# Kernel tuning notes

Measured on AMD Instinct MI355X. Metric: run time of the kernel, lower is better.

The kernel has to match this reference:

```python
import jax, jax.numpy as jnp
import numpy as np

NUM_HEADS = 12


def _apply_rope(t, cos, sin):
    # t: [B, N, H, Dh]; cos/sin: [N, Dh//2]
    B, N, H, Dh = t.shape
    tr = t.reshape(B, N, H, Dh // 2, 2)
    a, b = tr[..., 0], tr[..., 1]
    c = cos[None, :, None, :]
    s = sin[None, :, None, :]
    out_r = a * c - b * s
    out_i = a * s + b * c
    return jnp.stack([out_r, out_i], axis=-1).reshape(B, N, H, Dh)


def setup_inputs() -> dict:
    key = jax.random.key(0)
    ks = jax.random.split(key, 6)
    B, N, C, H = 4, 2048, 768, NUM_HEADS
    Dh = C // H
    x = jax.random.normal(ks[0], (B, N, C), dtype=jnp.float32)
    # RoPE frequencies (standard theta=10000 schedule) -> cos/sin of shape [N, Dh//2]
    inv_freq = 1.0 / (10000.0 ** (np.arange(0, Dh, 2, dtype=np.float32) / Dh))
    t = np.arange(N, dtype=np.float32)
    ang = np.outer(t, inv_freq)  # [N, Dh//2]
    freqs_cos = jnp.asarray(np.cos(ang))
    freqs_sin = jnp.asarray(np.sin(ang))
    # additive causal mask, broadcastable to [B, H, N, N]
    neg = jnp.float32(-1e9)
    mask = jnp.where(jnp.tril(jnp.ones((N, N), dtype=bool)), 0.0, neg)[None, None]
    w_qkv = jax.random.normal(ks[1], (3 * C, C), dtype=jnp.float32) * 0.02
    w_proj = jax.random.normal(ks[2], (C, C), dtype=jnp.float32) * 0.02
    b_proj = jnp.zeros((C,), dtype=jnp.float32)
    return {"x": x, "freqs_cos": freqs_cos, "freqs_sin": freqs_sin,
            "mask": mask, "w_qkv": w_qkv, "w_proj": w_proj, "b_proj": b_proj}


def reference(x, freqs_cos, freqs_sin, mask, w_qkv, w_proj, b_proj):
    B, N, C = x.shape
    H = NUM_HEADS
    Dh = C // H
    scale = Dh ** -0.5
    qkv = x @ w_qkv.T                               # [B, N, 3C] (qkv_bias=False)
    qkv = qkv.reshape(B, N, 3, H, Dh)
    q, k, v = qkv[:, :, 0], qkv[:, :, 1], qkv[:, :, 2]   # [B, N, H, Dh]
    q = _apply_rope(q, freqs_cos, freqs_sin)
    k = _apply_rope(k, freqs_cos, freqs_sin)
    q = q.transpose(0, 2, 1, 3)                     # [B, H, N, Dh]
    k = k.transpose(0, 2, 1, 3)
    v = v.transpose(0, 2, 1, 3)
    attn = jnp.einsum('bhqd,bhkd->bhqk', q, k) * scale
    attn = attn + mask
    attn = jax.nn.softmax(attn, axis=-1)
    out = jnp.einsum('bhqk,bhkd->bhqd', attn, v)    # [B, H, N, Dh]
    out = out.transpose(0, 2, 1, 3).reshape(B, N, C)
    return out @ w_proj.T + b_proj
```

## Files before the change

### kernel.cpp

```cpp
#include <hip/hip_runtime.h>
#include <hip/hip_bf16.h>

#define DEVI static __device__ __forceinline__

typedef __attribute__((ext_vector_type(8))) short bf16x8;
typedef __attribute__((ext_vector_type(4))) float f32x4;
typedef __attribute__((ext_vector_type(16))) float f32x16;
typedef __attribute__((ext_vector_type(4))) int i32x4;

constexpr int Bc = 4, Nc = 2048, Cc = 768, Hc = 12, Dhc = 64;
constexpr int Mc = Bc * Nc;
constexpr int K3c = 3 * Cc;

DEVI unsigned int f2bf(float f) {
  unsigned int u = __float_as_uint(f);
  return (u + 0x7fffu + ((u >> 16) & 1u)) >> 16;
}
DEVI float bf2f(unsigned int u) { return __uint_as_float(u << 16); }

DEVI unsigned int cvtpk_bf16(float lo, float hi_) {
  unsigned int r;
  asm("v_cvt_pk_bf16_f32 %0, %1, %2" : "=v"(r) : "v"(lo), "v"(hi_));
  return r;
}

#if __has_builtin(__builtin_amdgcn_exp2f)
#define EXP2(x) __builtin_amdgcn_exp2f(x)
#else
#define EXP2(x) exp2f(x)
#endif

#define GLOAD_LDS(g, l)                                                              \
  __builtin_amdgcn_global_load_lds((const __attribute__((address_space(1))) void*)(g), \
                                   (__attribute__((address_space(3))) void*)(l), 16, 0, 0)

DEVI unsigned int rope_pair(unsigned int w, float c, float s) {
  const float a = bf2f(w & 0xffffu), b_ = bf2f(w >> 16);
  return f2bf(a * c - b_ * s) | (f2bf(a * s + b_ * c) << 16);
}

__global__ __launch_bounds__(256) void cvt_f32_bf16(const float* __restrict__ in,
                                                    unsigned short* __restrict__ out, int n8) {
  const int i = blockIdx.x * 256 + threadIdx.x;
  if (i >= n8) return;
  const f32x4 a = *((const f32x4*)in + (size_t)i * 2);
  const f32x4 b = *((const f32x4*)in + (size_t)i * 2 + 1);
  i32x4 v;
  v.x = (int)(f2bf(a.x) | (f2bf(a.y) << 16));
  v.y = (int)(f2bf(a.z) | (f2bf(a.w) << 16));
  v.z = (int)(f2bf(b.x) | (f2bf(b.y) << 16));
  v.w = (int)(f2bf(b.z) | (f2bf(b.w) << 16));
  *((i32x4*)out + i) = v;
}

template <int OBF16>
__global__ __launch_bounds__(256) void gemm_bt16(const unsigned short* __restrict__ Ap,
                                                 const unsigned short* __restrict__ Wp,
                                                 void* __restrict__ Cp,
                                                 const float* __restrict__ bias,
                                                 int Nout, int Kdim) {
  __shared__ unsigned short As[128 * 64];
  __shared__ unsigned short Bs[128 * 64];
  const int tid = threadIdx.x;
  const int bn = blockIdx.x, bm = blockIdx.y;
  const int m0 = bm * 128, n0 = bn * 128;
  const int w = tid >> 6, lane = tid & 63;
  const int wr = w >> 1, wc = w & 1;
  const int lr = lane & 15, lg = lane >> 4;
  const int r = lane >> 3, slot = lane & 7;

  f32x4 acc[4][4];
#pragma unroll
  for (int i = 0; i < 4; ++i)
#pragma unroll
    for (int j = 0; j < 4; ++j) acc[i][j] = f32x4{0.f, 0.f, 0.f, 0.f};

  for (int kt = 0; kt < Kdim; kt += 64) {
    __syncthreads();
#pragma unroll
    for (int c = 0; c < 4; ++c) {
      const int i = (w << 2) + c;
      const int row = (i << 3) + r;
      const unsigned short* ga = Ap + (size_t)(m0 + row) * Kdim + kt + ((slot ^ r) << 3);
      GLOAD_LDS(ga, As + (i << 9));
      const unsigned short* gb = Wp + (size_t)(n0 + row) * Kdim + kt + ((slot ^ r) << 3);
      GLOAD_LDS(gb, Bs + (i << 9));
    }
    __syncthreads();

    bf16x8 af[4][2], bfr[4][2];
#pragma unroll
    for (int mf = 0; mf < 4; ++mf) {
      const int row = wr * 64 + mf * 16 + lr;
#pragma unroll
      for (int kk = 0; kk < 2; ++kk)
        af[mf][kk] = *(const bf16x8*)&As[row * 64 + (((kk * 4 + lg) ^ (row & 7)) * 8)];
    }
#pragma unroll
    for (int nf = 0; nf < 4; ++nf) {
      const int row = wc * 64 + nf * 16 + lr;
#pragma unroll
      for (int kk = 0; kk < 2; ++kk)
        bfr[nf][kk] = *(const bf16x8*)&Bs[row * 64 + (((kk * 4 + lg) ^ (row & 7)) * 8)];
    }
#pragma unroll
    for (int mf = 0; mf < 4; ++mf)
#pragma unroll
      for (int nf = 0; nf < 4; ++nf)
#pragma unroll
        for (int kk = 0; kk < 2; ++kk)
          acc[mf][nf] = __builtin_amdgcn_mfma_f32_16x16x32_bf16(af[mf][kk], bfr[nf][kk],
                                                                acc[mf][nf], 0, 0, 0);
  }

#pragma unroll
  for (int mf = 0; mf < 4; ++mf) {
#pragma unroll
    for (int nf = 0; nf < 4; ++nf) {
      const int col = n0 + wc * 64 + nf * 16 + lr;
#pragma unroll
      for (int rg = 0; rg < 4; ++rg) {
        const int rowg = m0 + wr * 64 + mf * 16 + lg * 4 + rg;
        const float v = acc[mf][nf][rg];
        if constexpr (OBF16) {
          ((unsigned short*)Cp)[(size_t)rowg * Nout + col] = (unsigned short)f2bf(v);
        } else {
          ((float*)Cp)[(size_t)rowg * Nout + col] = v + bias[col];
        }
      }
    }
  }
}

__global__ __launch_bounds__(256) void rope_q(const unsigned short* __restrict__ qkv,
                                              const float* __restrict__ fcos,
                                              const float* __restrict__ fsin,
                                              unsigned short* __restrict__ Qo) {
  constexpr float KL = 0.18033688011112042f;
  const int idx = blockIdx.x * 256 + threadIdx.x;
  if (idx >= Bc * Nc * Hc * 32) return;
  const int dp = idx & 31;
  const int t = idx >> 5;
  const int h = t % Hc;
  const int bn = t / Hc;
  const int n = bn & (Nc - 1);
  const int b = bn >> 11;
  const size_t qoff = (size_t)bn * 3 * Cc + h * 64 + dp * 2;
  const unsigned int qp = *(const unsigned int*)&qkv[qoff];
  const float c = fcos[n * 32 + dp], s = fsin[n * 32 + dp];
  const float qa = bf2f(qp & 0xffffu), qb = bf2f(qp >> 16);
  const unsigned int qo = f2bf(KL * (qa * c - qb * s)) | (f2bf(KL * (qa * s + qb * c)) << 16);
  const size_t o = ((size_t)((b * Hc + h) * Nc) + n) * Dhc + dp * 2;
  *(unsigned int*)&Qo[o] = qo;
}

__global__ __launch_bounds__(256) void pack_kv(const unsigned short* __restrict__ qkv,
                                               const float* __restrict__ fcos,
                                               const float* __restrict__ fsin,
                                               unsigned short* __restrict__ Kc,
                                               unsigned short* __restrict__ Vc) {
  __shared__ unsigned short kt[64 * 72];
  __shared__ unsigned short vt[64 * 72];
  const int nt = blockIdx.x, bh = blockIdx.y;
  const int b = bh / Hc, h = bh % Hc;
  const int n0 = nt * 64;
  const int tid = threadIdx.x;
  const int nl = tid >> 3, slot = tid & 7;

#pragma unroll
  for (int it = 0; it < 2; ++it) {
    const int n = it * 32 + nl;
    const size_t base = (size_t)(b * Nc + n0 + n) * K3c + h * 64 + slot * 8;
    i32x4 vv = *(const i32x4*)&qkv[base + 2 * Cc];
    *(i32x4*)&vt[n * 72 + slot * 8] = vv;
    i32x4 kv = *(const i32x4*)&qkv[base + Cc];
    const f32x4 cv = *(const f32x4*)&fcos[(n0 + n) * 32 + slot * 4];
    const f32x4 sv = *(const f32x4*)&fsin[(n0 + n) * 32 + slot * 4];
    i32x4 ko;
    ko.x = (int)rope_pair((unsigned int)kv.x, cv.x, sv.x);
    ko.y = (int)rope_pair((unsigned int)kv.y, cv.y, sv.y);
    ko.z = (int)rope_pair((unsigned int)kv.z, cv.z, sv.z);
    ko.w = (int)rope_pair((unsigned int)kv.w, cv.w, sv.w);
    *(i32x4*)&kt[n * 72 + slot * 8] = ko;
  }
  __syncthreads();

#pragma unroll
  for (int it = 0; it < 2; ++it) {
    const int task = it * 256 + tid;
    const int g = task >> 6;
    const int d = task & 63;
    unsigned short tmpv[8];
#pragma unroll
    for (int j = 0; j < 8; ++j) tmpv[j] = vt[(g * 8 + j) * 72 + d];
    *(i32x4*)&Vc[(((size_t)bh * 256 + (n0 >> 3) + g) * 64 + d) * 8] = *(const i32x4*)tmpv;
    *(i32x4*)&Kc[(((size_t)bh * 8 + g) * Nc + n0 + d) * 8] = *(const i32x4*)&kt[d * 72 + g * 8];
  }
}

__global__ __launch_bounds__(64, 4) void attn_fwd(const unsigned short* __restrict__ Qp,
                                                  const unsigned short* __restrict__ Kcp,
                                                  const unsigned short* __restrict__ Vcp,
                                                  unsigned short* __restrict__ Op) {
  const int id = blockIdx.x;
  const int x8 = id & 7;
  const int rr_ = id >> 3;
  const int seg = 63 - rr_ / 6;
  const int bh = x8 + ((rr_ % 6) << 3);
  const int lane = threadIdx.x;
  const int qc = lane & 31, hi = lane >> 5;
  const int qw0 = seg * 32;
  const int qrow = qw0 + qc;
  const int qwmax = qw0 + 31;
  const unsigned short* Kcb = Kcp + (size_t)bh * (8 * Nc * 8);
  const unsigned short* Vcb = Vcp + (size_t)bh * (256 * 64 * 8);

  bf16x8 qf[4];
  {
    const unsigned short* qptr = Qp + ((size_t)bh * Nc + qrow) * 64 + hi * 8;
#pragma unroll
    for (int ks = 0; ks < 4; ++ks) qf[ks] = *(const bf16x8*)(qptr + ks * 16);
  }

  f32x16 oacc[2];
#pragma unroll
  for (int dt = 0; dt < 2; ++dt)
#pragma unroll
    for (int j = 0; j < 16; ++j) oacc[dt][j] = 0.f;
  float m_run = -1e30f, l_run = 0.f;

  for (int k0 = 0; k0 <= qwmax; k0 += 64) {
    bf16x8 kf[2][4];
#pragma unroll
    for (int f = 0; f < 2; ++f)
#pragma unroll
      for (int ks = 0; ks < 4; ++ks)
        kf[f][ks] = *(const bf16x8*)&Kcb[(((2 * ks + hi) * Nc) + k0 + f * 32 + qc) * 8];

    bf16x8 vf[2][4];
#pragma unroll
    for (int dt = 0; dt < 2; ++dt)
#pragma unroll
      for (int ks = 0; ks < 4; ++ks)
        vf[dt][ks] = *(const bf16x8*)&Vcb[(((k0 >> 3) + 2 * ks + hi) * 64 + dt * 32 + qc) * 8];

    f32x16 sacc[2];
#pragma unroll
    for (int f = 0; f < 2; ++f)
#pragma unroll
      for (int j = 0; j < 16; ++j) sacc[f][j] = 0.f;
#pragma unroll
    for (int f = 0; f < 2; ++f)
#pragma unroll
      for (int ks = 0; ks < 4; ++ks)
        sacc[f] = __builtin_amdgcn_mfma_f32_32x32x16_bf16(kf[f][ks], qf[ks], sacc[f], 0, 0, 0);

    if (k0 + 63 > qw0) {
#pragma unroll
      for (int f = 0; f < 2; ++f)
#pragma unroll
        for (int rr = 0; rr < 16; ++rr) {
          const int kvi = k0 + f * 32 + (rr & 3) + ((rr >> 2) << 3) + (hi << 2);
          if (kvi > qrow) sacc[f][rr] = -1e30f;
        }
    }

    float mx[16];
#pragma unroll
    for (int j = 0; j < 16; ++j) mx[j] = fmaxf(sacc[0][j], sacc[1][j]);
#pragma unroll
    for (int st = 8; st >= 1; st >>= 1)
#pragma unroll
      for (int j = 0; j < st; ++j) mx[j] = fmaxf(mx[j], mx[j + st]);
    const float pmax = fmaxf(mx[0], __shfl_xor(mx[0], 32, 64));

    if (!__all(pmax - m_run <= 11.5f)) {
      const float m_new = fmaxf(m_run, pmax);
      const float rs = EXP2(m_run - m_new);
      l_run *= rs;
#pragma unroll
      for (int dt = 0; dt < 2; ++dt)
#pragma unroll
        for (int j = 0; j < 16; ++j) oacc[dt][j] *= rs;
      m_run = m_new;
    }

    float p[32];
#pragma unroll
    for (int f = 0; f < 2; ++f)
#pragma unroll
      for (int rr = 0; rr < 16; ++rr) p[f * 16 + rr] = EXP2(sacc[f][rr] - m_run);

    float ts[16];
#pragma unroll
    for (int j = 0; j < 16; ++j) ts[j] = p[j] + p[16 + j];
#pragma unroll
    for (int st = 8; st >= 1; st >>= 1)
#pragma unroll
      for (int j = 0; j < st; ++j) ts[j] += ts[j + st];
    l_run += ts[0] + __shfl_xor(ts[0], 32, 64);

    unsigned int pw[2][8];
#pragma unroll
    for (int f = 0; f < 2; ++f) {
#pragma unroll
      for (int j = 0; j < 8; ++j)
        pw[f][j] = cvtpk_bf16(p[f * 16 + 2 * j], p[f * 16 + 2 * j + 1]);
      asm volatile("v_permlane32_swap_b32 %0, %1" : "+v"(pw[f][0]), "+v"(pw[f][2]));
      asm volatile("v_permlane32_swap_b32 %0, %1" : "+v"(pw[f][1]), "+v"(pw[f][3]));
      asm volatile("v_permlane32_swap_b32 %0, %1" : "+v"(pw[f][4]), "+v"(pw[f][6]));
      asm volatile("v_permlane32_swap_b32 %0, %1" : "+v"(pw[f][5]), "+v"(pw[f][7]));
    }

#pragma unroll
    for (int dt = 0; dt < 2; ++dt)
#pragma unroll
      for (int ks = 0; ks < 4; ++ks) {
        i32x4 pi;
        pi.x = (int)pw[ks >> 1][(ks & 1) * 4 + 0];
        pi.y = (int)pw[ks >> 1][(ks & 1) * 4 + 1];
        pi.z = (int)pw[ks >> 1][(ks & 1) * 4 + 2];
        pi.w = (int)pw[ks >> 1][(ks & 1) * 4 + 3];
        bf16x8 pf = __builtin_bit_cast(bf16x8, pi);
        oacc[dt] = __builtin_amdgcn_mfma_f32_32x32x16_bf16(vf[dt][ks], pf, oacc[dt], 0, 0, 0);
      }
  }

  const float inv = 1.f / l_run;
  const int b = bh / Hc, h = bh % Hc;
  unsigned short* orow = Op + ((size_t)(b * Nc + qrow)) * Cc + h * 64;
#pragma unroll
  for (int dt = 0; dt < 2; ++dt)
#pragma unroll
    for (int rq = 0; rq < 4; ++rq) {
      const float o0 = oacc[dt][rq * 4 + 0] * inv;
      const float o1 = oacc[dt][rq * 4 + 1] * inv;
      const float o2 = oacc[dt][rq * 4 + 2] * inv;
      const float o3 = oacc[dt][rq * 4 + 3] * inv;
      uint2 val;
      val.x = f2bf(o0) | (f2bf(o1) << 16);
      val.y = f2bf(o2) | (f2bf(o3) << 16);
      *(uint2*)(orow + dt * 32 + rq * 8 + hi * 4) = val;
    }
}

extern "C" void kernel_launch(void* const* d_in, const int* in_sizes, int n_in,
                              void* d_out, int out_size, void* d_ws, size_t ws_size,
                              hipStream_t stream) {
  const float* x = (const float*)d_in[0];
  const float* fcos = (const float*)d_in[1];
  const float* fsin = (const float*)d_in[2];
  const float* wqkv = (const float*)d_in[4];
  const float* wproj = (const float*)d_in[5];
  const float* bproj = (const float*)d_in[6];

  char* ws = (char*)d_ws;
  unsigned short* qkvb = (unsigned short*)ws;
  unsigned short* Qb = (unsigned short*)(ws + 37748736);
  unsigned short* Kcb = (unsigned short*)(ws + 37748736 + 12582912);
  unsigned short* Vcb = (unsigned short*)(ws + 37748736 + 2 * 12582912);
  unsigned short* xb = Qb;
  unsigned short* wqkvb = Kcb;
  unsigned short* wprojb = Vcb;
  unsigned short* attnb = qkvb;

  cvt_f32_bf16<<<dim3(786432 / 256), 256, 0, stream>>>(x, xb, 786432);
  cvt_f32_bf16<<<dim3(221184 / 256), 256, 0, stream>>>(wqkv, wqkvb, 221184);
  gemm_bt16<1><<<dim3(K3c / 128, Mc / 128), 256, 0, stream>>>(xb, wqkvb, qkvb, nullptr,
                                                              K3c, Cc);
  rope_q<<<dim3(Bc * Nc * Hc * 32 / 256), 256, 0, stream>>>(qkvb, fcos, fsin, Qb);
  pack_kv<<<dim3(Nc / 64, Bc * Hc), 256, 0, stream>>>(qkvb, fcos, fsin, Kcb, Vcb);
  attn_fwd<<<dim3(3072), 64, 0, stream>>>(Qb, Kcb, Vcb, attnb);
  cvt_f32_bf16<<<dim3(73728 / 256), 256, 0, stream>>>(wproj, wprojb, 73728);
  gemm_bt16<0><<<dim3(Cc / 128, Mc / 128), 256, 0, stream>>>(attnb, wprojb, d_out, bproj,
                                                             Cc, Cc);
}
```

Measured before the change: 163.9 us.

## Pair short and long causal query tiles per wave to balance and share K/V loads

Each wave now handles two 32-row query tiles, one near the start and its mirror near the end of the sequence. It loads each K/V block once and applies it to both tiles, skipping the short tile once it passes the causal bound. Blocks now hold two waves, and the grid shrinks from 3072 to 768 blocks. The aim is to even out per-wave causal work and halve K/V fetches per query tile. In exchange it raises register pressure, since two sets of Q fragments and accumulators are live, which may lower occupancy.

```diff
diff --git a/kernel.cpp b/kernel.cpp
--- a/kernel.cpp
+++ b/kernel.cpp
@@ -198,45 +198,50 @@
   }
 }
 
-__global__ __launch_bounds__(64, 4) void attn_fwd(const unsigned short* __restrict__ Qp,
-                                                  const unsigned short* __restrict__ Kcp,
-                                                  const unsigned short* __restrict__ Vcp,
-                                                  unsigned short* __restrict__ Op) {
+__global__ __launch_bounds__(128) void attn_fwd(const unsigned short* __restrict__ Qp,
+                                                const unsigned short* __restrict__ Kcp,
+                                                const unsigned short* __restrict__ Vcp,
+                                                unsigned short* __restrict__ Op) {
   const int id = blockIdx.x;
   const int x8 = id & 7;
-  const int rr_ = id >> 3;
-  const int seg = 63 - rr_ / 6;
-  const int bh = x8 + ((rr_ % 6) << 3);
-  const int lane = threadIdx.x;
+  const int r_ = id >> 3;
+  const int t = r_ / 6;
+  const int bh = x8 + ((r_ % 6) << 3);
+  const int wv = threadIdx.x >> 6, lane = threadIdx.x & 63;
   const int qc = lane & 31, hi = lane >> 5;
-  const int qw0 = seg * 32;
-  const int qrow = qw0 + qc;
-  const int qwmax = qw0 + 31;
+  const int sA = 2 * t + wv;
+  const int qA0 = sA * 32, qB0 = (63 - sA) * 32;
+  const int qrowA = qA0 + qc, qrowB = qB0 + qc;
   const unsigned short* Kcb = Kcp + (size_t)bh * (8 * Nc * 8);
   const unsigned short* Vcb = Vcp + (size_t)bh * (256 * 64 * 8);
 
-  bf16x8 qf[4];
+  bf16x8 qfA[4], qfB[4];
   {
-    const unsigned short* qptr = Qp + ((size_t)bh * Nc + qrow) * 64 + hi * 8;
-#pragma unroll
-    for (int ks = 0; ks < 4; ++ks) qf[ks] = *(const bf16x8*)(qptr + ks * 16);
-  }
-
-  f32x16 oacc[2];
+    const unsigned short* qpA = Qp + ((size_t)bh * Nc + qrowA) * 64 + hi * 8;
+    const unsigned short* qpB = Qp + ((size_t)bh * Nc + qrowB) * 64 + hi * 8;
+#pragma unroll
+    for (int ks = 0; ks < 4; ++ks) {
+      qfA[ks] = *(const bf16x8*)(qpA + ks * 16);
+      qfB[ks] = *(const bf16x8*)(qpB + ks * 16);
+    }
+  }
+
+  f32x16 oaccA[2], oaccB[2];
 #pragma unroll
   for (int dt = 0; dt < 2; ++dt)
 #pragma unroll
-    for (int j = 0; j < 16; ++j) oacc[dt][j] = 0.f;
-  float m_run = -1e30f, l_run = 0.f;
-
-  for (int k0 = 0; k0 <= qwmax; k0 += 64) {
+    for (int j = 0; j < 16; ++j) { oaccA[dt][j] = 0.f; oaccB[dt][j] = 0.f; }
+  float mA = -1e30f, lA = 0.f, mB = -1e30f, lB = 0.f;
+
+  for (int k0 = 0; k0 <= qB0 + 31; k0 += 64) {
+    const bool actA = (k0 <= qA0 + 31);
+
     bf16x8 kf[2][4];
 #pragma unroll
     for (int f = 0; f < 2; ++f)
 #pragma unroll
       for (int ks = 0; ks < 4; ++ks)
         kf[f][ks] = *(const bf16x8*)&Kcb[(((2 * ks + hi) * Nc) + k0 + f * 32 + qc) * 8];
-
     bf16x8 vf[2][4];
 #pragma unroll
     for (int dt = 0; dt < 2; ++dt)
@@ -244,104 +249,194 @@
       for (int ks = 0; ks < 4; ++ks)
         vf[dt][ks] = *(const bf16x8*)&Vcb[(((k0 >> 3) + 2 * ks + hi) * 64 + dt * 32 + qc) * 8];
 
-    f32x16 sacc[2];
-#pragma unroll
-    for (int f = 0; f < 2; ++f)
-#pragma unroll
-      for (int j = 0; j < 16; ++j) sacc[f][j] = 0.f;
-#pragma unroll
-    for (int f = 0; f < 2; ++f)
-#pragma unroll
-      for (int ks = 0; ks < 4; ++ks)
-        sacc[f] = __builtin_amdgcn_mfma_f32_32x32x16_bf16(kf[f][ks], qf[ks], sacc[f], 0, 0, 0);
-
-    if (k0 + 63 > qw0) {
-#pragma unroll
-      for (int f = 0; f < 2; ++f)
-#pragma unroll
-        for (int rr = 0; rr < 16; ++rr) {
-          const int kvi = k0 + f * 32 + (rr & 3) + ((rr >> 2) << 3) + (hi << 2);
-          if (kvi > qrow) sacc[f][rr] = -1e30f;
+    {
+      f32x16 sacc[2];
+#pragma unroll
+      for (int f = 0; f < 2; ++f)
+#pragma unroll
+        for (int j = 0; j < 16; ++j) sacc[f][j] = 0.f;
+#pragma unroll
+      for (int f = 0; f < 2; ++f)
+#pragma unroll
+        for (int ks = 0; ks < 4; ++ks)
+          sacc[f] = __builtin_amdgcn_mfma_f32_32x32x16_bf16(kf[f][ks], qfB[ks], sacc[f], 0, 0, 0);
+
+      if (k0 + 63 > qB0) {
+#pragma unroll
+        for (int f = 0; f < 2; ++f)
+#pragma unroll
+          for (int rr = 0; rr < 16; ++rr) {
+            const int kvi = k0 + f * 32 + (rr & 3) + ((rr >> 2) << 3) + (hi << 2);
+            if (kvi > qrowB) sacc[f][rr] = -1e30f;
+          }
+      }
+
+      float mx[16];
+#pragma unroll
+      for (int j = 0; j < 16; ++j) mx[j] = fmaxf(sacc[0][j], sacc[1][j]);
+#pragma unroll
+      for (int st = 8; st >= 1; st >>= 1)
+#pragma unroll
+        for (int j = 0; j < st; ++j) mx[j] = fmaxf(mx[j], mx[j + st]);
+      const float pmax = fmaxf(mx[0], __shfl_xor(mx[0], 32, 64));
+      if (!__all(pmax - mB <= 11.5f)) {
+        const float m_new = fmaxf(mB, pmax);
+        const float rs = EXP2(mB - m_new);
+        lB *= rs;
+#pragma unroll
+        for (int dt = 0; dt < 2; ++dt)
+#pragma unroll
+          for (int j = 0; j < 16; ++j) oaccB[dt][j] *= rs;
+        mB = m_new;
+      }
+
+      float p[32];
+#pragma unroll
+      for (int f = 0; f < 2; ++f)
+#pragma unroll
+        for (int rr = 0; rr < 16; ++rr) p[f * 16 + rr] = EXP2(sacc[f][rr] - mB);
+      float ts[16];
+#pragma unroll
+      for (int j = 0; j < 16; ++j) ts[j] = p[j] + p[16 + j];
+#pragma unroll
+      for (int st = 8; st >= 1; st >>= 1)
+#pragma unroll
+        for (int j = 0; j < st; ++j) ts[j] += ts[j + st];
+      lB += ts[0] + __shfl_xor(ts[0], 32, 64);
+
+      unsigned int pw[2][8];
+#pragma unroll
+      for (int f = 0; f < 2; ++f) {
+#pragma unroll
+        for (int j = 0; j < 8; ++j)
+          pw[f][j] = cvtpk_bf16(p[f * 16 + 2 * j], p[f * 16 + 2 * j + 1]);
+        asm volatile("v_permlane32_swap_b32 %0, %1" : "+v"(pw[f][0]), "+v"(pw[f][2]));
+        asm volatile("v_permlane32_swap_b32 %0, %1" : "+v"(pw[f][1]), "+v"(pw[f][3]));
+        asm volatile("v_permlane32_swap_b32 %0, %1" : "+v"(pw[f][4]), "+v"(pw[f][6]));
+        asm volatile("v_permlane32_swap_b32 %0, %1" : "+v"(pw[f][5]), "+v"(pw[f][7]));
+      }
+#pragma unroll
+      for (int dt = 0; dt < 2; ++dt)
+#pragma unroll
+        for (int ks = 0; ks < 4; ++ks) {
+          i32x4 pi;
+          pi.x = (int)pw[ks >> 1][(ks & 1) * 4 + 0];
+          pi.y = (int)pw[ks >> 1][(ks & 1) * 4 + 1];
+          pi.z = (int)pw[ks >> 1][(ks & 1) * 4 + 2];
+          pi.w = (int)pw[ks >> 1][(ks & 1) * 4 + 3];
+          bf16x8 pf = __builtin_bit_cast(bf16x8, pi);
+          oaccB[dt] = __builtin_amdgcn_mfma_f32_32x32x16_bf16(vf[dt][ks], pf, oaccB[dt], 0, 0, 0);
         }
     }
 
-    float mx[16];
-#pragma unroll
-    for (int j = 0; j < 16; ++j) mx[j] = fmaxf(sacc[0][j], sacc[1][j]);
-#pragma unroll
-    for (int st = 8; st >= 1; st >>= 1)
-#pragma unroll
-      for (int j = 0; j < st; ++j) mx[j] = fmaxf(mx[j], mx[j + st]);
-    const float pmax = fmaxf(mx[0], __shfl_xor(mx[0], 32, 64));
-
-    if (!__all(pmax - m_run <= 11.5f)) {
-      const float m_new = fmaxf(m_run, pmax);
-      const float rs = EXP2(m_run - m_new);
-      l_run *= rs;
+    if (actA) {
+      f32x16 sacc[2];
+#pragma unroll
+      for (int f = 0; f < 2; ++f)
+#pragma unroll
+        for (int j = 0; j < 16; ++j) sacc[f][j] = 0.f;
+#pragma unroll
+      for (int f = 0; f < 2; ++f)
+#pragma unroll
+        for (int ks = 0; ks < 4; ++ks)
+          sacc[f] = __builtin_amdgcn_mfma_f32_32x32x16_bf16(kf[f][ks], qfA[ks], sacc[f], 0, 0, 0);
+
+      if (k0 + 63 > qA0) {
+#pragma unroll
+        for (int f = 0; f < 2; ++f)
+#pragma unroll
+          for (int rr = 0; rr < 16; ++rr) {
+            const int kvi = k0 + f * 32 + (rr & 3) + ((rr >> 2) << 3) + (hi << 2);
+            if (kvi > qrowA) sacc[f][rr] = -1e30f;
+          }
+      }
+
+      float mx[16];
+#pragma unroll
+      for (int j = 0; j < 16; ++j) mx[j] = fmaxf(sacc[0][j], sacc[1][j]);
+#pragma unroll
+      for (int st = 8; st >= 1; st >>= 1)
+#pragma unroll
+        for (int j = 0; j < st; ++j) mx[j] = fmaxf(mx[j], mx[j + st]);
+      const float pmax = fmaxf(mx[0], __shfl_xor(mx[0], 32, 64));
+      if (!__all(pmax - mA <= 11.5f)) {
+        const float m_new = fmaxf(mA, pmax);
+        const float rs = EXP2(mA - m_new);
+        lA *= rs;
+#pragma unroll
+        for (int dt = 0; dt < 2; ++dt)
+#pragma unroll
+          for (int j = 0; j < 16; ++j) oaccA[dt][j] *= rs;
+        mA = m_new;
+      }
+
+      float p[32];
+#pragma unroll
+      for (int f = 0; f < 2; ++f)
+#pragma unroll
+        for (int rr = 0; rr < 16; ++rr) p[f * 16 + rr] = EXP2(sacc[f][rr] - mA);
+      float ts[16];
+#pragma unroll
+      for (int j = 0; j < 16; ++j) ts[j] = p[j] + p[16 + j];
+#pragma unroll
+      for (int st = 8; st >= 1; st >>= 1)
+#pragma unroll
+        for (int j = 0; j < st; ++j) ts[j] += ts[j + st];
+      lA += ts[0] + __shfl_xor(ts[0], 32, 64);
+
+      unsigned int pw[2][8];
+#pragma unroll
+      for (int f = 0; f < 2; ++f) {
+#pragma unroll
+        for (int j = 0; j < 8; ++j)
+          pw[f][j] = cvtpk_bf16(p[f * 16 + 2 * j], p[f * 16 + 2 * j + 1]);
+        asm volatile("v_permlane32_swap_b32 %0, %1" : "+v"(pw[f][0]), "+v"(pw[f][2]));
+        asm volatile("v_permlane32_swap_b32 %0, %1" : "+v"(pw[f][1]), "+v"(pw[f][3]));
+        asm volatile("v_permlane32_swap_b32 %0, %1" : "+v"(pw[f][4]), "+v"(pw[f][6]));
+        asm volatile("v_permlane32_swap_b32 %0, %1" : "+v"(pw[f][5]), "+v"(pw[f][7]));
+      }
 #pragma unroll
       for (int dt = 0; dt < 2; ++dt)
 #pragma unroll
-        for (int j = 0; j < 16; ++j) oacc[dt][j] *= rs;
-      m_run = m_new;
-    }
-
-    float p[32];
-#pragma unroll
-    for (int f = 0; f < 2; ++f)
-#pragma unroll
-      for (int rr = 0; rr < 16; ++rr) p[f * 16 + rr] = EXP2(sacc[f][rr] - m_run);
-
-    float ts[16];
-#pragma unroll
-    for (int j = 0; j < 16; ++j) ts[j] = p[j] + p[16 + j];
-#pragma unroll
-    for (int st = 8; st >= 1; st >>= 1)
-#pragma unroll
-      for (int j = 0; j < st; ++j) ts[j] += ts[j + st];
-    l_run += ts[0] + __shfl_xor(ts[0], 32, 64);
-
-    unsigned int pw[2][8];
-#pragma unroll
-    for (int f = 0; f < 2; ++f) {
-#pragma unroll
-      for (int j = 0; j < 8; ++j)
-        pw[f][j] = cvtpk_bf16(p[f * 16 + 2 * j], p[f * 16 + 2 * j + 1]);
-      asm volatile("v_permlane32_swap_b32 %0, %1" : "+v"(pw[f][0]), "+v"(pw[f][2]));
-      asm volatile("v_permlane32_swap_b32 %0, %1" : "+v"(pw[f][1]), "+v"(pw[f][3]));
-      asm volatile("v_permlane32_swap_b32 %0, %1" : "+v"(pw[f][4]), "+v"(pw[f][6]));
-      asm volatile("v_permlane32_swap_b32 %0, %1" : "+v"(pw[f][5]), "+v"(pw[f][7]));
-    }
-
+        for (int ks = 0; ks < 4; ++ks) {
+          i32x4 pi;
+          pi.x = (int)pw[ks >> 1][(ks & 1) * 4 + 0];
+          pi.y = (int)pw[ks >> 1][(ks & 1) * 4 + 1];
+          pi.z = (int)pw[ks >> 1][(ks & 1) * 4 + 2];
+          pi.w = (int)pw[ks >> 1][(ks & 1) * 4 + 3];
+          bf16x8 pf = __builtin_bit_cast(bf16x8, pi);
+          oaccA[dt] = __builtin_amdgcn_mfma_f32_32x32x16_bf16(vf[dt][ks], pf, oaccA[dt], 0, 0, 0);
+        }
+    }
+  }
+
+  const int b = bh / Hc, h = bh % Hc;
+  {
+    const float inv = 1.f / lA;
+    unsigned short* orow = Op + ((size_t)(b * Nc + qrowA)) * Cc + h * 64;
 #pragma unroll
     for (int dt = 0; dt < 2; ++dt)
 #pragma unroll
-      for (int ks = 0; ks < 4; ++ks) {
-        i32x4 pi;
-        pi.x = (int)pw[ks >> 1][(ks & 1) * 4 + 0];
-        pi.y = (int)pw[ks >> 1][(ks & 1) * 4 + 1];
-        pi.z = (int)pw[ks >> 1][(ks & 1) * 4 + 2];
-        pi.w = (int)pw[ks >> 1][(ks & 1) * 4 + 3];
-        bf16x8 pf = __builtin_bit_cast(bf16x8, pi);
-        oacc[dt] = __builtin_amdgcn_mfma_f32_32x32x16_bf16(vf[dt][ks], pf, oacc[dt], 0, 0, 0);
-      }
-  }
-
-  const float inv = 1.f / l_run;
-  const int b = bh / Hc, h = bh % Hc;
-  unsigned short* orow = Op + ((size_t)(b * Nc + qrow)) * Cc + h * 64;
-#pragma unroll
-  for (int dt = 0; dt < 2; ++dt)
-#pragma unroll
-    for (int rq = 0; rq < 4; ++rq) {
-      const float o0 = oacc[dt][rq * 4 + 0] * inv;
-      const float o1 = oacc[dt][rq * 4 + 1] * inv;
-      const float o2 = oacc[dt][rq * 4 + 2] * inv;
-      const float o3 = oacc[dt][rq * 4 + 3] * inv;
-      uint2 val;
-      val.x = f2bf(o0) | (f2bf(o1) << 16);
-      val.y = f2bf(o2) | (f2bf(o3) << 16);
-      *(uint2*)(orow + dt * 32 + rq * 8 + hi * 4) = val;
-    }
+      for (int rq = 0; rq < 4; ++rq) {
+        uint2 val;
+        val.x = f2bf(oaccA[dt][rq * 4 + 0] * inv) | (f2bf(oaccA[dt][rq * 4 + 1] * inv) << 16);
+        val.y = f2bf(oaccA[dt][rq * 4 + 2] * inv) | (f2bf(oaccA[dt][rq * 4 + 3] * inv) << 16);
+        *(uint2*)(orow + dt * 32 + rq * 8 + hi * 4) = val;
+      }
+  }
+  {
+    const float inv = 1.f / lB;
+    unsigned short* orow = Op + ((size_t)(b * Nc + qrowB)) * Cc + h * 64;
+#pragma unroll
+    for (int dt = 0; dt < 2; ++dt)
+#pragma unroll
+      for (int rq = 0; rq < 4; ++rq) {
+        uint2 val;
+        val.x = f2bf(oaccB[dt][rq * 4 + 0] * inv) | (f2bf(oaccB[dt][rq * 4 + 1] * inv) << 16);
+        val.y = f2bf(oaccB[dt][rq * 4 + 2] * inv) | (f2bf(oaccB[dt][rq * 4 + 3] * inv) << 16);
+        *(uint2*)(orow + dt * 32 + rq * 8 + hi * 4) = val;
+      }
+  }
 }
 
 extern "C" void kernel_launch(void* const* d_in, const int* in_sizes, int n_in,
@@ -370,7 +465,7 @@
                                                               K3c, Cc);
   rope_q<<<dim3(Bc * Nc * Hc * 32 / 256), 256, 0, stream>>>(qkvb, fcos, fsin, Qb);
   pack_kv<<<dim3(Nc / 64, Bc * Hc), 256, 0, stream>>>(qkvb, fcos, fsin, Kcb, Vcb);
-  attn_fwd<<<dim3(3072), 64, 0, stream>>>(Qb, Kcb, Vcb, attnb);
+  attn_fwd<<<dim3(768), 128, 0, stream>>>(Qb, Kcb, Vcb, attnb);
   cvt_f32_bf16<<<dim3(73728 / 256), 256, 0, stream>>>(wproj, wprojb, 73728);
   gemm_bt16<0><<<dim3(Cc / 128, Mc / 128), 256, 0, stream>>>(attnb, wprojb, d_out, bproj,
                                                              Cc, Cc);
```

After: 170.8 us. 4.2% more time.
